# Kernel tuning notes

Hardware: AMD Instinct MI355X
Metric: run time of the kernel (lower is better)

## Reference

```python
import jax, jax.numpy as jnp
import numpy as np

B, CIN, COUT, WDIM, RES, K = 16, 512, 512, 512, 64, 3
LRELU_SLOPE = 0.2
ACT_GAIN = np.sqrt(2.0).astype(np.float32)  # def_gain for 'lrelu'


def setup_inputs() -> dict:
    key = jax.random.key(0)
    ks = jax.random.split(key, 7)
    return {
        "x": jax.random.normal(ks[0], (B, CIN, RES, RES), dtype=jnp.float32),
        "w": jax.random.normal(ks[1], (B, WDIM), dtype=jnp.float32),
        "weight": jax.random.normal(ks[2], (COUT, CIN, K, K), dtype=jnp.float32),
        "affine_w": jax.random.normal(ks[3], (CIN, WDIM), dtype=jnp.float32),
        "affine_b": jnp.ones((CIN,), dtype=jnp.float32),  # bias_init=1
        "bias": jnp.zeros((COUT,), dtype=jnp.float32),
        "noise_const": jax.random.normal(ks[4], (RES, RES), dtype=jnp.float32),
        "noise_strength": jnp.float32(0.1),
    }


def reference(x, w, weight, affine_w, affine_b, bias, noise_const, noise_strength):
    # affine: FullyConnectedLayer with weight_gain = 1/sqrt(w_dim)
    wg = jnp.float32(1.0 / np.sqrt(WDIM))
    styles = w @ (affine_w * wg).T + affine_b  # [B, CIN]

    # fused modulated conv2d (demodulate=True, fused_modconv=True, up=down=1)
    wm = weight[None] * styles[:, None, :, None, None]  # [B, COUT, CIN, K, K]
    dcoefs = jax.lax.rsqrt(jnp.sum(wm * wm, axis=(2, 3, 4)) + 1e-8)  # [B, COUT]
    wm = wm * dcoefs[:, :, None, None, None]

    # grouped conv trick: groups = batch
    xg = x.reshape(1, B * CIN, RES, RES)
    wgk = wm.reshape(B * COUT, CIN, K, K)
    pad = K // 2
    y = jax.lax.conv_general_dilated(
        xg, wgk, window_strides=(1, 1), padding=[(pad, pad), (pad, pad)],
        dimension_numbers=("NCHW", "OIHW", "NCHW"), feature_group_count=B,
    ).reshape(B, COUT, RES, RES)

    # const noise injection
    y = y + noise_const * noise_strength

    # bias_act: bias + leaky_relu + gain (conv_clamp=None, gain=1.0)
    y = jax.nn.leaky_relu(y + bias[None, :, None, None], LRELU_SLOPE) * ACT_GAIN
    return y
```

## Files before the change

kernel.cpp:

```cpp
#include <hip/hip_runtime.h>

#define BATCH 16
#define CIN 512
#define COUT 512
#define RES 64
#define K_TILES 72

typedef __attribute__((ext_vector_type(8))) short bf16x8;
typedef __attribute__((ext_vector_type(4))) float f32x4;

__device__ __align__(16) unsigned short g_zero[64];

static __device__ __forceinline__ unsigned short f2bf(float f) {
    unsigned int u = __float_as_uint(f);
    u += 0x7fffu + ((u >> 16) & 1u);
    return (unsigned short)(u >> 16);
}

static __device__ __forceinline__ void gload16(const void* g, void* l) {
    __builtin_amdgcn_global_load_lds(
        (const __attribute__((address_space(1))) void*)g,
        (__attribute__((address_space(3))) void*)l, 16, 0, 0);
}

__global__ void k_prep1(const float* __restrict__ w, const float* __restrict__ aw,
                        const float* __restrict__ ab, const float* __restrict__ weight,
                        float* __restrict__ styles, unsigned short* __restrict__ wA,
                        float* __restrict__ wsq) {
    if (blockIdx.x < 2048) {
        int wid  = (blockIdx.x * blockDim.x + threadIdx.x) >> 6;
        int lane = threadIdx.x & 63;
        int b = wid >> 9, i = wid & 511;
        const float* wrow = w + b * 512;
        const float* arow = aw + (size_t)i * 512;
        float acc = 0.f;
        for (int k = lane; k < 512; k += 64) acc += wrow[k] * arow[k];
        for (int off = 32; off; off >>= 1) acc += __shfl_down(acc, off, 64);
        if (lane == 0) styles[wid] = acc * 0.04419417382415922f + ab[i];
    } else {
        int o = blockIdx.x - 2048;
        __shared__ float lw[4608];
        for (int idx = threadIdx.x; idx < 4608; idx += 256)
            lw[idx] = weight[(size_t)o * 4608 + idx];
        __syncthreads();
        int i = threadIdx.x * 2;
        float sq0 = 0.f, sq1 = 0.f;
#pragma unroll
        for (int t = 0; t < 9; ++t) {
            float v0 = lw[i * 9 + t], v1 = lw[(i + 1) * 9 + t];
            sq0 += v0 * v0; sq1 += v1 * v1;
            unsigned* dst = (unsigned*)(wA + (((size_t)t * COUT + o) << 9));
            dst[threadIdx.x] = (unsigned)f2bf(v0) | ((unsigned)f2bf(v1) << 16);
        }
        *(float2*)(wsq + ((size_t)o << 9) + i) = make_float2(sq0, sq1);
    }
}

__global__ void k_dcoefs(const float* __restrict__ wsq, const float* __restrict__ styles,
                         float* __restrict__ dcoefs) {
    int wid  = (blockIdx.x * blockDim.x + threadIdx.x) >> 6;
    int lane = threadIdx.x & 63;
    int b = wid >> 9, o = wid & 511;
    const float* srow = styles + b * 512;
    const float* qrow = wsq + ((size_t)o << 9);
    float acc = 0.f;
    for (int i = lane; i < 512; i += 64) {
        float s = srow[i];
        acc += s * s * qrow[i];
    }
    for (int off = 32; off; off >>= 1) acc += __shfl_down(acc, off, 64);
    if (lane == 0) dcoefs[wid] = rsqrtf(acc + 1e-8f);
}

__global__ __launch_bounds__(512) void k_xpose(const float* __restrict__ x,
                                               const float* __restrict__ styles,
                                               unsigned short* __restrict__ xt) {
    int bh = blockIdx.x;
    int b = bh >> 6, h = bh & 63;
    __shared__ float tile[512][65];
    __shared__ float st[512];
    const int tid = threadIdx.x;
    st[tid] = styles[b * 512 + tid];
    __syncthreads();
    const float* src = x + ((size_t)b * 512) * 4096 + h * 64;
#pragma unroll
    for (int it = 0; it < 16; ++it) {
        int idx = it * 512 + tid;
        int c = idx >> 4, w4 = (idx & 15) * 4;
        float4 v = *(const float4*)(src + (size_t)c * 4096 + w4);
        float s = st[c];
        tile[c][w4] = v.x * s; tile[c][w4 + 1] = v.y * s;
        tile[c][w4 + 2] = v.z * s; tile[c][w4 + 3] = v.w * s;
    }
    __syncthreads();
    const int w = tid >> 3, l3 = tid & 7;
    unsigned short* outp = xt + (((size_t)bh * 64 + w) << 9) + l3 * 64;
#pragma unroll
    for (int g = 0; g < 8; ++g) {
        int bb = (g ^ l3) * 8;
        int c0 = l3 * 64 + bb;
        unsigned pk0 = (unsigned)f2bf(tile[c0 + 0][w]) | ((unsigned)f2bf(tile[c0 + 1][w]) << 16);
        unsigned pk1 = (unsigned)f2bf(tile[c0 + 2][w]) | ((unsigned)f2bf(tile[c0 + 3][w]) << 16);
        unsigned pk2 = (unsigned)f2bf(tile[c0 + 4][w]) | ((unsigned)f2bf(tile[c0 + 5][w]) << 16);
        unsigned pk3 = (unsigned)f2bf(tile[c0 + 6][w]) | ((unsigned)f2bf(tile[c0 + 7][w]) << 16);
        *(uint4*)(outp + bb) = make_uint4(pk0, pk1, pk2, pk3);
    }
}

__global__ __launch_bounds__(512, 2)
void k_conv(const unsigned short* __restrict__ wA, const unsigned short* __restrict__ xt,
            const float* __restrict__ dcoefs,
            const float* __restrict__ noise, const float* __restrict__ nstr,
            const float* __restrict__ bias, float* __restrict__ out) {
    __shared__ __align__(16) unsigned short lA[2][16384];
    __shared__ __align__(16) unsigned short lB[2][16384];
    __shared__ float sdc[256];
    __shared__ float sbias[256];

    const int tid  = threadIdx.x;
    const int lane = tid & 63;
    const int wave = tid >> 6;
    const int wm = wave >> 2;
    const int wn = wave & 3;

    const int orig  = blockIdx.x;
    const int wgid  = (orig & 7) * 64 + (orig >> 3);
    const int o_blk = wgid & 1;
    const int ptile = wgid >> 1;
    const int b     = ptile >> 4;
    const int h0    = (ptile & 15) << 2;
    const int o0    = o_blk * 256;
    const int p0    = (ptile & 15) << 8;

    const int srow  = tid >> 3;
    const int qsrc8 = ((tid & 7) ^ (srow & 7)) * 8;

    const int l7 = lane & 7;
    const int a_off = (wm * 128 + (lane & 15)) * 128;
    const int b_off = (wn * 64  + (lane & 15)) * 128;
    const int qk0 = (((lane >> 4)    ) ^ l7) * 16;
    const int qk1 = (((lane >> 4) | 4) ^ l7) * 16;

    const unsigned short* pA;
    const unsigned short* pB[4];
    int aB[4];

    auto recompA = [&](int ktt) {
        pA = wA + (((size_t)((ktt >> 3) * COUT + o0 + srow)) << 9)
                + ((ktt & 7) << 6) + qsrc8;
    };
    auto recompB = [&](int ktt) {
        int tap = ktt >> 3;
        int ty = tap / 3;
        int dy = ty - 1, dx = tap - ty * 3 - 1;
        int wv = srow + dx;
        bool wok = (unsigned)wv < 64u;
        int i0 = (ktt & 7) << 6;
#pragma unroll
        for (int s = 0; s < 4; ++s) {
            int hh = h0 + s + dy;
            bool ok = wok && ((unsigned)hh < 64u);
            pB[s] = ok ? xt + (((size_t)(b * 4096 + hh * 64 + wv)) << 9) + i0 + qsrc8
                       : g_zero + qsrc8;
            aB[s] = ok ? 64 : 0;
        }
    };
    auto stageA = [&](int d) {
        char* lb = (char*)&lA[d][0] + wave * 1024;
        gload16(pA,               lb);
        gload16(pA + (64  << 9),  lb + 8192);
        gload16(pA + (128 << 9),  lb + 16384);
        gload16(pA + (192 << 9),  lb + 24576);
    };
    auto stageB = [&](int d) {
        char* lb = (char*)&lB[d][0] + wave * 1024;
        gload16(pB[0], lb);
        gload16(pB[1], lb + 8192);
        gload16(pB[2], lb + 16384);
        gload16(pB[3], lb + 24576);
    };

    bf16x8 afr[2][4], bfr[2][4];
    f32x4 acc[8][4];
#pragma unroll
    for (int i = 0; i < 8; ++i)
#pragma unroll
        for (int j = 0; j < 4; ++j) acc[i][j] = (f32x4){0.f, 0.f, 0.f, 0.f};

#define RD_A(S, H, QK, BASE) do {                                            \
    afr[S][0] = *(const bf16x8*)((BASE) + a_off + ((H)*4 + 0)*2048 + (QK));  \
    afr[S][1] = *(const bf16x8*)((BASE) + a_off + ((H)*4 + 1)*2048 + (QK));  \
    afr[S][2] = *(const bf16x8*)((BASE) + a_off + ((H)*4 + 2)*2048 + (QK));  \
    afr[S][3] = *(const bf16x8*)((BASE) + a_off + ((H)*4 + 3)*2048 + (QK));  \
} while (0)
#define RD_B(S, QK, BASE) do {                                               \
    bfr[S][0] = *(const bf16x8*)((BASE) + b_off + 0*2048 + (QK));            \
    bfr[S][1] = *(const bf16x8*)((BASE) + b_off + 1*2048 + (QK));            \
    bfr[S][2] = *(const bf16x8*)((BASE) + b_off + 2*2048 + (QK));            \
    bfr[S][3] = *(const bf16x8*)((BASE) + b_off + 3*2048 + (QK));            \
} while (0)
#define MM(AS, BS, H) do {                                                   \
    _Pragma("unroll")                                                        \
    for (int _j = 0; _j < 4; ++_j) {                                         \
        _Pragma("unroll")                                                    \
        for (int _fn = 0; _fn < 4; ++_fn)                                    \
            acc[(H)*4 + _j][_fn] = __builtin_amdgcn_mfma_f32_16x16x32_bf16(  \
                afr[AS][_j], bfr[BS][_fn], acc[(H)*4 + _j][_fn], 0, 0, 0);   \
    }                                                                        \
} while (0)

    recompA(0); recompB(0); stageA(0); stageB(0);
    recompA(1); recompB(1); stageA(1); stageB(1);
    recompA(2); recompB(2);
    asm volatile("s_waitcnt vmcnt(8)" ::: "memory");
    __builtin_amdgcn_s_barrier();
    {
        const char* bA0 = (const char*)&lA[0][0];
        const char* bB0 = (const char*)&lB[0][0];
        RD_A(0, 0, qk0, bA0);
        RD_B(0, qk0, bB0);
    }

    for (int kt = 0; kt < K_TILES; ++kt) {
        const int cur = kt & 1;
        const char* bA = (const char*)&lA[cur][0];
        const char* bB = (const char*)&lB[cur][0];
        const char* nA = (const char*)&lA[cur ^ 1][0];
        const char* nB = (const char*)&lB[cur ^ 1][0];

        RD_A(1, 1, qk0, bA);
        __builtin_amdgcn_sched_barrier(0);
        __builtin_amdgcn_s_setprio(1);
        MM(0, 0, 0);
        __builtin_amdgcn_s_setprio(0);

        RD_A(0, 0, qk1, bA);
        RD_B(1, qk1, bB);
        __builtin_amdgcn_sched_barrier(0);
        __builtin_amdgcn_s_setprio(1);
        MM(1, 0, 1);
        __builtin_amdgcn_s_setprio(0);

        RD_A(1, 1, qk1, bA);
        __builtin_amdgcn_sched_barrier(0);
        __builtin_amdgcn_s_setprio(1);
        MM(0, 1, 0);
        __builtin_amdgcn_s_setprio(0);
        asm volatile("s_waitcnt lgkmcnt(0)" ::: "memory");
        __builtin_amdgcn_s_barrier();

        if (kt + 2 < K_TILES) {
            stageA(cur); stageB(cur);
            int nk = kt + 3;
            if (nk < K_TILES) {
                if ((nk & 7) == 0) { recompA(nk); recompB(nk); }
                else {
                    pA += 64;
                    pB[0] += aB[0]; pB[1] += aB[1]; pB[2] += aB[2]; pB[3] += aB[3];
                }
            }
            asm volatile("s_waitcnt vmcnt(8)" ::: "memory");
        } else {
            asm volatile("s_waitcnt vmcnt(0)" ::: "memory");
        }
        __builtin_amdgcn_s_barrier();
        if (kt + 1 < K_TILES) {
            RD_A(0, 0, qk0, nA);
            RD_B(0, qk0, nB);
        }
        __builtin_amdgcn_sched_barrier(0);
        __builtin_amdgcn_s_setprio(1);
        MM(1, 1, 1);
        __builtin_amdgcn_s_setprio(0);
    }

    if (tid < 256) {
        sdc[tid]   = dcoefs[b * 512 + o0 + tid];
        sbias[tid] = bias[o0 + tid];
    }
    __syncthreads();
    const float ns = nstr[0];
    const int prow = (lane >> 4) * 4;
#pragma unroll
    for (int fm = 0; fm < 8; ++fm) {
        const int ob = wm * 128 + fm * 16 + prow;
#pragma unroll
        for (int fn = 0; fn < 4; ++fn) {
            const int p = p0 + wn * 64 + fn * 16 + (lane & 15);
            const float nv = noise[p] * ns;
#pragma unroll
            for (int rg = 0; rg < 4; ++rg) {
                const int oo = ob + rg;
                float v = acc[fm][fn][rg] * sdc[oo] + nv + sbias[oo];
                v = (v > 0.f ? v : 0.2f * v) * 1.41421356f;
                out[((size_t)(b * COUT + o0 + oo) << 12) + p] = v;
            }
        }
    }
#undef RD_A
#undef RD_B
#undef MM
}

__global__ void k_conv_naive(const float* __restrict__ x, const float* __restrict__ w,
                             const float* __restrict__ weight,
                             const float* __restrict__ aw, const float* __restrict__ ab,
                             const float* __restrict__ noise, const float* __restrict__ nstr,
                             const float* __restrict__ bias, float* __restrict__ out) {
    const int o = blockIdx.x, b = blockIdx.y;
    __shared__ float ss[512];
    __shared__ float red[256];
    const float* wv = w + b * 512;
    for (int i = threadIdx.x; i < 512; i += 256) {
        const float* arow = aw + (size_t)i * 512;
        float acc = 0.f;
        for (int k = 0; k < 512; ++k) acc += wv[k] * arow[k];
        ss[i] = acc * 0.04419417382415922f + ab[i];
    }
    __syncthreads();
    float part = 0.f;
    for (int i = threadIdx.x; i < 512; i += 256) {
        float s = ss[i], sq = 0.f;
#pragma unroll
        for (int k = 0; k < 9; ++k) { float v = weight[((size_t)o * 512 + i) * 9 + k]; sq += v * v; }
        part += s * s * sq;
    }
    red[threadIdx.x] = part;
    __syncthreads();
    for (int st = 128; st; st >>= 1) {
        if (threadIdx.x < st) red[threadIdx.x] += red[threadIdx.x + st];
        __syncthreads();
    }
    const float dcoef = rsqrtf(red[0] + 1e-8f);

    float acc[16];
#pragma unroll
    for (int j = 0; j < 16; ++j) acc[j] = 0.f;
    for (int i = 0; i < 512; ++i) {
        const float s = ss[i];
        float wk[9];
#pragma unroll
        for (int k = 0; k < 9; ++k) wk[k] = weight[((size_t)o * 512 + i) * 9 + k] * s;
        const float* xp = x + ((size_t)b * 512 + i) * 4096;
#pragma unroll
        for (int j = 0; j < 16; ++j) {
            const int p = (j << 8) + threadIdx.x;
            const int h = p >> 6, ww = p & 63;
            float a = acc[j];
#pragma unroll
            for (int ky = 0; ky < 3; ++ky) {
                int hh = h + ky - 1;
                if ((unsigned)hh < 64u) {
#pragma unroll
                    for (int kx = 0; kx < 3; ++kx) {
                        int wv2 = ww + kx - 1;
                        if ((unsigned)wv2 < 64u) a += wk[ky * 3 + kx] * xp[hh * 64 + wv2];
                    }
                }
            }
            acc[j] = a;
        }
    }
    const float ns = nstr[0], bs = bias[o];
#pragma unroll
    for (int j = 0; j < 16; ++j) {
        int p = (j << 8) + threadIdx.x;
        float v = acc[j] * dcoef + noise[p] * ns + bs;
        v = (v > 0.f ? v : 0.2f * v) * 1.41421356f;
        out[((size_t)(b * COUT + o) << 12) + p] = v;
    }
}

extern "C" void kernel_launch(void* const* d_in, const int* in_sizes, int n_in,
                              void* d_out, int out_size, void* d_ws, size_t ws_size,
                              hipStream_t stream) {
    const float* x   = (const float*)d_in[0];
    const float* w   = (const float*)d_in[1];
    const float* wt  = (const float*)d_in[2];
    const float* aw  = (const float*)d_in[3];
    const float* ab  = (const float*)d_in[4];
    const float* bs  = (const float*)d_in[5];
    const float* nc  = (const float*)d_in[6];
    const float* nst = (const float*)d_in[7];
    float* out = (float*)d_out;

    char* ws = (char*)d_ws;
    float* styles = (float*)ws;
    float* dcoefs = (float*)(ws + 32 * 1024);
    float* wsq    = (float*)(ws + 64 * 1024);
    unsigned short* wA = (unsigned short*)(ws + (2 << 20));
    unsigned short* xt = (unsigned short*)(ws + (2 << 20) + 4718592ull);
    const size_t need = (size_t)(2 << 20) + 4718592ull + 67108864ull;

    if (d_ws != nullptr && ws_size >= need) {
        k_prep1<<<2560, 256, 0, stream>>>(w, aw, ab, wt, styles, wA, wsq);
        k_dcoefs<<<2048, 256, 0, stream>>>(wsq, styles, dcoefs);
        k_xpose<<<1024, 512, 0, stream>>>(x, styles, xt);
        k_conv<<<512, 512, 0, stream>>>(wA, xt, dcoefs, nc, nst, bs, out);
    } else {
        k_conv_naive<<<dim3(512, 16), 256, 0, stream>>>(x, w, wt, aw, ab, nc, nst, bs, out);
    }
}
```

Baseline: 538.8 us.

## Interleave LDS reads with MFMAs via sched_group_barrier and peel final K tiles

Replaces the hard sched_barrier fences between LDS fragment reads and MFMA blocks with sched_group_barrier patterns that interleave one ds_read with two or four MFMAs. The goal is to hide LDS latency behind matrix work. The last two K iterations are peeled out of the main loop, which drops the per-iteration branches on staging and the conditional next-tile reads. The risk is that fragment reads are consumed before they arrive, or that the compiler's scheduling ends up worse than the manual fences.

```diff
diff --git a/kernel.cpp b/kernel.cpp
--- a/kernel.cpp
+++ b/kernel.cpp
@@ -208,6 +208,16 @@
                 afr[AS][_j], bfr[BS][_fn], acc[(H)*4 + _j][_fn], 0, 0, 0);   \
     }                                                                        \
 } while (0)
+#define SGB_R1M4 do { _Pragma("unroll")                                      \
+    for (int _u = 0; _u < 4; ++_u) {                                         \
+        __builtin_amdgcn_sched_group_barrier(0x100, 1, 0);                   \
+        __builtin_amdgcn_sched_group_barrier(0x008, 4, 0);                   \
+    } } while (0)
+#define SGB_R1M2 do { _Pragma("unroll")                                      \
+    for (int _u = 0; _u < 8; ++_u) {                                         \
+        __builtin_amdgcn_sched_group_barrier(0x100, 1, 0);                   \
+        __builtin_amdgcn_sched_group_barrier(0x008, 2, 0);                   \
+    } } while (0)
 
     recompA(0); recompB(0); stageA(0); stageB(0);
     recompA(1); recompB(1); stageA(1); stageB(1);
@@ -221,36 +231,37 @@
         RD_B(0, qk0, bB0);
     }
 
-    for (int kt = 0; kt < K_TILES; ++kt) {
+    for (int kt = 0; kt < K_TILES - 2; ++kt) {
         const int cur = kt & 1;
         const char* bA = (const char*)&lA[cur][0];
         const char* bB = (const char*)&lB[cur][0];
         const char* nA = (const char*)&lA[cur ^ 1][0];
         const char* nB = (const char*)&lB[cur ^ 1][0];
 
+        __builtin_amdgcn_s_setprio(1);
         RD_A(1, 1, qk0, bA);
-        __builtin_amdgcn_sched_barrier(0);
+        MM(0, 0, 0);
+        SGB_R1M4;
+        __builtin_amdgcn_s_setprio(0);
+
         __builtin_amdgcn_s_setprio(1);
-        MM(0, 0, 0);
-        __builtin_amdgcn_s_setprio(0);
-
         RD_A(0, 0, qk1, bA);
         RD_B(1, qk1, bB);
-        __builtin_amdgcn_sched_barrier(0);
+        MM(1, 0, 1);
+        SGB_R1M2;
+        __builtin_amdgcn_s_setprio(0);
+
         __builtin_amdgcn_s_setprio(1);
-        MM(1, 0, 1);
+        RD_A(1, 1, qk1, bA);
+        MM(0, 1, 0);
+        SGB_R1M4;
         __builtin_amdgcn_s_setprio(0);
 
-        RD_A(1, 1, qk1, bA);
-        __builtin_amdgcn_sched_barrier(0);
-        __builtin_amdgcn_s_setprio(1);
-        MM(0, 1, 0);
-        __builtin_amdgcn_s_setprio(0);
         asm volatile("s_waitcnt lgkmcnt(0)" ::: "memory");
         __builtin_amdgcn_s_barrier();
 
-        if (kt + 2 < K_TILES) {
-            stageA(cur); stageB(cur);
+        stageA(cur); stageB(cur);
+        {
             int nk = kt + 3;
             if (nk < K_TILES) {
                 if ((nk & 7) == 0) { recompA(nk); recompB(nk); }
@@ -259,19 +270,37 @@
                     pB[0] += aB[0]; pB[1] += aB[1]; pB[2] += aB[2]; pB[3] += aB[3];
                 }
             }
-            asm volatile("s_waitcnt vmcnt(8)" ::: "memory");
-        } else {
-            asm volatile("s_waitcnt vmcnt(0)" ::: "memory");
         }
+        asm volatile("s_waitcnt vmcnt(8)" ::: "memory");
         __builtin_amdgcn_s_barrier();
-        if (kt + 1 < K_TILES) {
-            RD_A(0, 0, qk0, nA);
-            RD_B(0, qk0, nB);
-        }
-        __builtin_amdgcn_sched_barrier(0);
+
         __builtin_amdgcn_s_setprio(1);
+        RD_A(0, 0, qk0, nA);
+        RD_B(0, qk0, nB);
         MM(1, 1, 1);
+        SGB_R1M2;
         __builtin_amdgcn_s_setprio(0);
+    }
+
+    {
+        const char* bA = (const char*)&lA[0][0];
+        const char* bB = (const char*)&lB[0][0];
+        const char* nA = (const char*)&lA[1][0];
+        const char* nB = (const char*)&lB[1][0];
+        RD_A(1, 1, qk0, bA); MM(0, 0, 0);
+        RD_A(0, 0, qk1, bA); RD_B(1, qk1, bB); MM(1, 0, 1);
+        RD_A(1, 1, qk1, bA); MM(0, 1, 0);
+        asm volatile("s_waitcnt vmcnt(0)" ::: "memory");
+        __builtin_amdgcn_s_barrier();
+        RD_A(0, 0, qk0, nA); RD_B(0, qk0, nB); MM(1, 1, 1);
+    }
+    {
+        const char* bA = (const char*)&lA[1][0];
+        const char* bB = (const char*)&lB[1][0];
+        RD_A(1, 1, qk0, bA); MM(0, 0, 0);
+        RD_A(0, 0, qk1, bA); RD_B(1, qk1, bB); MM(1, 0, 1);
+        RD_A(1, 1, qk1, bA); MM(0, 1, 0);
+        MM(1, 1, 1);
     }
 
     if (tid < 256) {
@@ -300,6 +329,8 @@
 #undef RD_A
 #undef RD_B
 #undef MM
+#undef SGB_R1M4
+#undef SGB_R1M2
 }
 
 __global__ void k_conv_naive(const float* __restrict__ x, const float* __restrict__ w,
```

New measurement: 526.0 us. 2.4% less time.
